# Performance work log

Measured on AMD Instinct MI355X. Metric: run time of the kernel, lower is better.

Reference implementation:

```python
import jax, jax.numpy as jnp
import numpy as np

N_NODES = 80000
N_EDGES = 1280000
IN_CH = 128
OUT_CH = 32
HID = 2 * OUT_CH


def gcn_conv(x, W, b, src, dst, n_nodes):
    """PyG GCNConv with self-loops and symmetric normalization.
    out[i] = b + sum_{j->i} deg(j)^-1/2 deg(i)^-1/2 (x_j @ W)
    """
    loop = jnp.arange(n_nodes, dtype=src.dtype)
    s = jnp.concatenate([src, loop])  # [E+N]
    d = jnp.concatenate([dst, loop])  # [E+N]
    deg = jax.ops.segment_sum(jnp.ones_like(d, dtype=x.dtype), d,
                              num_segments=n_nodes)  # in-degree incl. self loop
    dinv = jnp.where(deg > 0, jax.lax.rsqrt(deg), 0.0)
    norm = dinv[s] * dinv[d]  # [E+N]
    h = x @ W  # [N, F_out] dense transform first (fewer flops when F_out < F_in)
    msg = h[s] * norm[:, None]  # [E+N, F_out] gather + scale
    out = jax.ops.segment_sum(msg, d, num_segments=n_nodes)  # scatter-add
    return out + b


def setup_inputs() -> dict:
    key = jax.random.key(0)
    k1, k2, k3, k4 = jax.random.split(key, 4)
    x = jax.random.normal(k1, (N_NODES, IN_CH), dtype=jnp.float32)
    edge_index = jax.random.randint(k2, (2, N_EDGES), 0, N_NODES, dtype=jnp.int64)
    W1 = jax.random.normal(k3, (IN_CH, HID), dtype=jnp.float32) / np.sqrt(IN_CH)
    b1 = jnp.zeros((HID,), dtype=jnp.float32)
    W2 = jax.random.normal(k4, (HID, OUT_CH), dtype=jnp.float32) / np.sqrt(HID)
    b2 = jnp.zeros((OUT_CH,), dtype=jnp.float32)
    return {"x": x, "edge_index": edge_index, "W1": W1, "b1": b1,
            "W2": W2, "b2": b2}


def reference(x, edge_index, W1, b1, W2, b2):
    src, dst = edge_index[0], edge_index[1]
    h = jax.nn.relu(gcn_conv(x, W1, b1, src, dst, N_NODES))
    return gcn_conv(h, W2, b2, src, dst, N_NODES)
```

## Files before the change

### kernel.cpp

```cpp
#include <hip/hip_runtime.h>
#include <hip/hip_fp16.h>

#define N_NODES 80000
#define N_EDGES 1280000
#define IN_CH 128
#define HID 64
#define OUT_CH 32

#define NBUCK 625
#define CAP 3072
#define BIN_BLOCKS 256

typedef float vf2 __attribute__((ext_vector_type(2)));
typedef float vf4 __attribute__((ext_vector_type(4)));
typedef short short8 __attribute__((ext_vector_type(8)));
typedef float floatx4 __attribute__((ext_vector_type(4)));

__device__ __forceinline__ unsigned bf16rn(float x) {
    unsigned u = __float_as_uint(x);
    return (u + 0x7FFFu + ((u >> 16) & 1u)) >> 16;
}
__device__ __forceinline__ unsigned packbf2(float a, float b) {
    return bf16rn(a) | (bf16rn(b) << 16);
}
__device__ __forceinline__ float hl(unsigned u) {
    return __half2float(__ushort_as_half((unsigned short)(u & 0xFFFFu)));
}
__device__ __forceinline__ float hh(unsigned u) {
    return __half2float(__ushort_as_half((unsigned short)(u >> 16)));
}
__device__ __forceinline__ unsigned pack2h(float a, float b) {
    return (unsigned)__half_as_ushort(__float2half_rn(a)) |
           ((unsigned)__half_as_ushort(__float2half_rn(b)) << 16);
}

__global__ __launch_bounds__(256) void k_bin_gemm1(
        const int* __restrict__ src, const int* __restrict__ dst,
        int* __restrict__ gcur, unsigned int* __restrict__ binned,
        const float* __restrict__ x, const float* __restrict__ W1,
        unsigned short* __restrict__ h1h) {
    __shared__ unsigned short smem_u[26112];
    int bid = blockIdx.x, t = threadIdx.x;
    if (bid < BIN_BLOCKS) {
        int* hist = (int*)smem_u;
        int* lcur = hist + NBUCK;
        const int chunk = N_EDGES / BIN_BLOCKS;
        int e0 = bid * chunk;
        int e1 = e0 + chunk;
        for (int i = t; i < NBUCK; i += 256) hist[i] = 0;
        __syncthreads();
        for (int e = e0 + t; e < e1; e += 256)
            atomicAdd(&hist[dst[e] >> 7], 1);
        __syncthreads();
        for (int i = t; i < NBUCK; i += 256) {
            int h = hist[i];
            lcur[i] = h ? atomicAdd(&gcur[i], h) : 0;
        }
        __syncthreads();
        for (int e = e0 + t; e < e1; e += 256) {
            int d = dst[e];
            int bk = d >> 7;
            int pos = atomicAdd(&lcur[bk], 1);
            if (pos < CAP)
                binned[(size_t)bk * CAP + pos] =
                    (unsigned int)src[e] | ((unsigned int)(d & 127) << 17);
        }
    } else {
        unsigned short* sX = smem_u;
        unsigned short* sWT = smem_u + 128 * 136;
        long long nb = (long long)(bid - BIN_BLOCKS) * 128;
        for (int it = 0; it < 16; ++it) {
            int idx = t + it * 256;
            int node = idx >> 5, k4 = (idx & 31) * 4;
            float4 v = *(const float4*)&x[(nb + node) * IN_CH + k4];
            unsigned u0 = packbf2(v.x, v.y), u1 = packbf2(v.z, v.w);
            *(uint2*)&sX[node * 136 + k4] = (uint2){u0, u1};
        }
        for (int it = 0; it < 8; ++it) {
            int idx = t + it * 256;
            int k = idx >> 4, c4 = (idx & 15) * 4;
            float4 w = *(const float4*)&W1[k * 64 + c4];
            sWT[(c4 + 0) * 136 + k] = (unsigned short)bf16rn(w.x);
            sWT[(c4 + 1) * 136 + k] = (unsigned short)bf16rn(w.y);
            sWT[(c4 + 2) * 136 + k] = (unsigned short)bf16rn(w.z);
            sWT[(c4 + 3) * 136 + k] = (unsigned short)bf16rn(w.w);
        }
        __syncthreads();
        int wv = t >> 6, lane = t & 63;
        int lm = lane & 15, q = lane >> 4;
        int m0 = wv * 32;
        floatx4 acc[2][4];
#pragma unroll
        for (int i = 0; i < 2; ++i)
#pragma unroll
            for (int j = 0; j < 4; ++j) acc[i][j] = (floatx4){0.f, 0.f, 0.f, 0.f};
#pragma unroll
        for (int kk = 0; kk < 128; kk += 32) {
            short8 a0 = *(short8*)&sX[(m0 + lm) * 136 + kk + q * 8];
            short8 a1 = *(short8*)&sX[(m0 + 16 + lm) * 136 + kk + q * 8];
#pragma unroll
            for (int ct = 0; ct < 4; ++ct) {
                short8 bfr = *(short8*)&sWT[(ct * 16 + lm) * 136 + kk + q * 8];
                acc[0][ct] = __builtin_amdgcn_mfma_f32_16x16x32_bf16(a0, bfr, acc[0][ct], 0, 0, 0);
                acc[1][ct] = __builtin_amdgcn_mfma_f32_16x16x32_bf16(a1, bfr, acc[1][ct], 0, 0, 0);
            }
        }
#pragma unroll
        for (int mt = 0; mt < 2; ++mt)
#pragma unroll
            for (int ct = 0; ct < 4; ++ct)
#pragma unroll
                for (int r = 0; r < 4; ++r) {
                    long long node = nb + m0 + mt * 16 + q * 4 + r;
                    int c = ct * 16 + lm;
                    h1h[node * 64 + c] = __half_as_ushort(__float2half_rn(acc[mt][ct][r]));
                }
    }
}

__global__ __launch_bounds__(256) void k_csr(const unsigned int* __restrict__ binned,
                                             const int* __restrict__ cnt,
                                             int* __restrict__ csr,
                                             int2* __restrict__ rse,
                                             float* __restrict__ dinv,
                                             unsigned int* __restrict__ h1u) {
    __shared__ int deg[128];
    __shared__ int scan[128];
    __shared__ int cur[128];
    __shared__ float sdinv[128];
    int bk = blockIdx.x, t = threadIdx.x;
    int n_e = min(cnt[bk], CAP);
    const unsigned int* eb = binned + (size_t)bk * CAP;
    if (t < 128) deg[t] = 0;
    __syncthreads();
    for (int i = t; i < n_e; i += 256) atomicAdd(&deg[eb[i] >> 17], 1);
    __syncthreads();
    if (t < 128) scan[t] = deg[t];
    __syncthreads();
    for (int off = 1; off < 128; off <<= 1) {
        int v = (t < 128 && t >= off) ? scan[t - off] : 0;
        __syncthreads();
        if (t < 128) scan[t] += v;
        __syncthreads();
    }
    if (t < 128) {
        int incl = scan[t];
        int s = incl - deg[t];
        cur[t] = s;
        int n = bk * 128 + t;
        int base = bk * CAP;
        rse[n] = make_int2(base + s, base + incl);
        float dv = rsqrtf((float)(deg[t] + 1));
        dinv[n] = dv;
        sdinv[t] = dv;
    }
    __syncthreads();
    if (t < 32) {
        int p = n_e + t;
        if (p < CAP) csr[(size_t)bk * CAP + p] = 0;
    }
    for (int i = t; i < n_e; i += 256) {
        unsigned int p = eb[i];
        int dL = p >> 17;
        int pos = atomicAdd(&cur[dL], 1);
        csr[bk * CAP + pos] = (int)(p & 0x1FFFF);
    }
    size_t rbase = (size_t)bk * 128 * 32;
    for (int i = t; i < 128 * 16; i += 256) {
        int row = i >> 4, c = i & 15;
        uint2 u = *(uint2*)&h1u[rbase + (size_t)row * 32 + 2 * c];
        float dv = sdinv[row];
        u.x = pack2h(dv * hl(u.x), dv * hh(u.x));
        u.y = pack2h(dv * hl(u.y), dv * hh(u.y));
        *(uint2*)&h1u[rbase + (size_t)row * 32 + 2 * c] = u;
    }
}

__global__ __launch_bounds__(256) void k_agg64(
        const unsigned int* __restrict__ h1u, const int* __restrict__ csr,
        const int2* __restrict__ rse, const float* __restrict__ dinv,
        const float* __restrict__ b1, const float* __restrict__ W2,
        unsigned int* __restrict__ g2u) {
    __shared__ float sW2[64 * 32];
    __shared__ float sH2[4][2][64];
    int t = threadIdx.x;
    for (int i = t * 2; i < 64 * 32; i += 512)
        *(vf2*)&sW2[i] = *(const vf2*)&W2[i];

    int wv = t >> 6, lane = t & 63;
    int nd = lane >> 5;
    int q  = (lane >> 4) & 1;
    int fo = lane & 15;
    int col = lane & 31;
    int n = blockIdx.x * 8 + wv * 2 + nd;

    int2 rb = rse[n];
    float dn = dinv[n];
    uint2 un = *(const uint2*)&h1u[(size_t)n * 32 + 2 * fo];
    float4 bb = *(const float4*)&b1[4 * fo];
    int a = rb.x, b = rb.y;
    int e0 = a + q;
    int ss[12];
#pragma unroll
    for (int i = 0; i < 12; ++i) ss[i] = csr[e0 + 2 * i];
#pragma unroll
    for (int i = 1; i < 12; ++i) ss[i] = (e0 + 2 * i < b) ? ss[i] : ss[0];
    float ax = 0.f, ay = 0.f, az = 0.f, aw = 0.f;
#pragma unroll
    for (int i = 0; i < 12; ++i) {
        uint2 u = *(const uint2*)&h1u[(size_t)ss[i] * 32 + 2 * fo];
        if (e0 + 2 * i < b) {
            ax += hl(u.x); ay += hh(u.x); az += hl(u.y); aw += hh(u.y);
        }
    }
    for (int e = e0 + 24; e < b; e += 2) {
        int s = csr[e];
        uint2 u = *(const uint2*)&h1u[(size_t)s * 32 + 2 * fo];
        ax += hl(u.x); ay += hh(u.x); az += hl(u.y); aw += hh(u.y);
    }
    ax += __shfl_down(ax, 16); ay += __shfl_down(ay, 16);
    az += __shfl_down(az, 16); aw += __shfl_down(aw, 16);
    __syncthreads();
    if (q == 0) {
        ax += hl(un.x); ay += hh(un.x); az += hl(un.y); aw += hh(un.y);
        vf4 h2v = {fmaxf(dn * ax + bb.x, 0.f), fmaxf(dn * ay + bb.y, 0.f),
                   fmaxf(dn * az + bb.z, 0.f), fmaxf(dn * aw + bb.w, 0.f)};
        *(vf4*)&sH2[wv][nd][4 * fo] = h2v;
    }
    __syncthreads();
    int nd2 = lane >> 5;
    const float* hrow = sH2[wv][nd2];
    float g = 0.f;
#pragma unroll
    for (int k = 0; k < 64; ++k) g += hrow[k] * sW2[k * 32 + col];
    g *= dn;
    float g1 = __shfl_down(g, 1);
    float g2v = __shfl_down(g, 2);
    float g3v = __shfl_down(g, 3);
    if ((lane & 3) == 0) {
        uint2 p = {pack2h(g, g1), pack2h(g2v, g3v)};
        *(uint2*)&g2u[(size_t)n * 16 + (col >> 1)] = p;
    }
}

__global__ __launch_bounds__(256) void k_agg32(
        const unsigned int* __restrict__ g2u, const int* __restrict__ csr,
        const int2* __restrict__ rse, const float* __restrict__ dinv,
        const float* __restrict__ b2, float* __restrict__ outp) {
    int n = blockIdx.x * 4 + (threadIdx.x >> 6);
    int lane = threadIdx.x & 63;
    int oc = lane >> 3, fo = lane & 7;
    int2 rb = rse[n];
    float dn = dinv[n];
    uint2 un = *(const uint2*)&g2u[(size_t)n * 16 + 2 * fo];
    int a = rb.x, b = rb.y;
    int e0 = a + oc;
    int s0 = csr[e0];
    int s1 = csr[e0 + 8];
    int s2 = csr[e0 + 16];
    s1 = (e0 + 8  < b) ? s1 : s0;
    s2 = (e0 + 16 < b) ? s2 : s0;
    float ax = 0.f, ay = 0.f, az = 0.f, aw = 0.f;
    uint2 u0 = *(const uint2*)&g2u[(size_t)s0 * 16 + 2 * fo];
    uint2 u1 = *(const uint2*)&g2u[(size_t)s1 * 16 + 2 * fo];
    uint2 u2 = *(const uint2*)&g2u[(size_t)s2 * 16 + 2 * fo];
    if (e0 < b)      { ax += hl(u0.x); ay += hh(u0.x); az += hl(u0.y); aw += hh(u0.y); }
    if (e0 + 8 < b)  { ax += hl(u1.x); ay += hh(u1.x); az += hl(u1.y); aw += hh(u1.y); }
    if (e0 + 16 < b) { ax += hl(u2.x); ay += hh(u2.x); az += hl(u2.y); aw += hh(u2.y); }
    for (int e = e0 + 24; e < b; e += 8) {
        int s = csr[e];
        uint2 u = *(const uint2*)&g2u[(size_t)s * 16 + 2 * fo];
        ax += hl(u.x); ay += hh(u.x); az += hl(u.y); aw += hh(u.y);
    }
    ax += __shfl_down(ax, 32); ay += __shfl_down(ay, 32);
    az += __shfl_down(az, 32); aw += __shfl_down(aw, 32);
    ax += __shfl_down(ax, 16); ay += __shfl_down(ay, 16);
    az += __shfl_down(az, 16); aw += __shfl_down(aw, 16);
    ax += __shfl_down(ax, 8);  ay += __shfl_down(ay, 8);
    az += __shfl_down(az, 8);  aw += __shfl_down(aw, 8);
    if (oc == 0) {
        ax += hl(un.x); ay += hh(un.x);
        az += hl(un.y); aw += hh(un.y);
        float4 bbv = *(const float4*)&b2[4 * fo];
        vf4 o = {dn * ax + bbv.x, dn * ay + bbv.y, dn * az + bbv.z, dn * aw + bbv.w};
        __builtin_nontemporal_store(o, (vf4*)&outp[(size_t)n * 32 + 4 * fo]);
    }
}

static inline size_t align256(size_t x) { return (x + 255) & ~(size_t)255; }

extern "C" void kernel_launch(void* const* d_in, const int* in_sizes, int n_in,
                              void* d_out, int out_size, void* d_ws, size_t ws_size,
                              hipStream_t stream) {
    const float* x  = (const float*)d_in[0];
    const int*   ei = (const int*)d_in[1];
    const float* W1 = (const float*)d_in[2];
    const float* b1 = (const float*)d_in[3];
    const float* W2 = (const float*)d_in[4];
    const float* b2 = (const float*)d_in[5];
    float* out = (float*)d_out;

    const int* src = ei;
    const int* dst = ei + N_EDGES;

    char* ws = (char*)d_ws;
    size_t off = 0;
    int* gcur = (int*)(ws + off);              off = align256(off + NBUCK * 4);
    unsigned int* binned = (unsigned int*)(ws + off);
                                               off = align256(off + (size_t)NBUCK * CAP * 4);
    int* csr = (int*)(ws + off);               off = align256(off + (size_t)NBUCK * CAP * 4 + 128);
    int2* rse = (int2*)(ws + off);             off = align256(off + (size_t)N_NODES * 8);
    float* dinv = (float*)(ws + off);          off = align256(off + (size_t)N_NODES * 4);
    unsigned short* h1h = (unsigned short*)(ws + off);
                                               off = align256(off + (size_t)N_NODES * 64 * 2);
    unsigned int* g2u = (unsigned int*)(ws + off);
                                               off = align256(off + (size_t)N_NODES * 16 * 4);

    (void)hipMemsetAsync(gcur, 0, NBUCK * 4, stream);
    k_bin_gemm1<<<BIN_BLOCKS + N_NODES / 128, 256, 0, stream>>>(src, dst, gcur, binned,
                                                                x, W1, h1h);
    k_csr<<<NBUCK, 256, 0, stream>>>(binned, gcur, csr, rse, dinv,
                                     (unsigned int*)h1h);
    k_agg64<<<N_NODES / 8, 256, 0, stream>>>((const unsigned int*)h1h, csr, rse,
                                             dinv, b1, W2, g2u);
    k_agg32<<<N_NODES / 4, 256, 0, stream>>>(g2u, csr, rse, dinv, b2, out);
}
```

Measured before the change: 202.0 us.

## Add padded ELL neighbor table with zero sentinel row for aggregation kernels

```diff
diff --git a/kernel.cpp b/kernel.cpp
--- a/kernel.cpp
+++ b/kernel.cpp
@@ -10,6 +10,7 @@
 #define NBUCK 625
 #define CAP 3072
 #define BIN_BLOCKS 256
+#define ELLW 24
 
 typedef float vf2 __attribute__((ext_vector_type(2)));
 typedef float vf4 __attribute__((ext_vector_type(4)));
@@ -121,12 +122,14 @@
 __global__ __launch_bounds__(256) void k_csr(const unsigned int* __restrict__ binned,
                                              const int* __restrict__ cnt,
                                              int* __restrict__ csr,
+                                             int* __restrict__ ell,
                                              int2* __restrict__ rse,
-                                             float* __restrict__ dinv,
+                                             float2* __restrict__ meta,
                                              unsigned int* __restrict__ h1u) {
     __shared__ int deg[128];
     __shared__ int scan[128];
     __shared__ int cur[128];
+    __shared__ int rst[128];
     __shared__ float sdinv[128];
     int bk = blockIdx.x, t = threadIdx.x;
     int n_e = min(cnt[bk], CAP);
@@ -147,23 +150,25 @@
         int incl = scan[t];
         int s = incl - deg[t];
         cur[t] = s;
+        rst[t] = s;
         int n = bk * 128 + t;
         int base = bk * CAP;
         rse[n] = make_int2(base + s, base + incl);
         float dv = rsqrtf((float)(deg[t] + 1));
-        dinv[n] = dv;
+        meta[n] = make_float2(dv, (float)deg[t]);
         sdinv[t] = dv;
     }
-    __syncthreads();
-    if (t < 32) {
-        int p = n_e + t;
-        if (p < CAP) csr[(size_t)bk * CAP + p] = 0;
-    }
+    int* eb_ell = ell + (size_t)bk * 128 * ELLW;
+    for (int i = t; i < 128 * ELLW; i += 256) eb_ell[i] = N_NODES;
+    __syncthreads();
     for (int i = t; i < n_e; i += 256) {
         unsigned int p = eb[i];
         int dL = p >> 17;
         int pos = atomicAdd(&cur[dL], 1);
-        csr[bk * CAP + pos] = (int)(p & 0x1FFFF);
+        int s = (int)(p & 0x1FFFF);
+        csr[bk * CAP + pos] = s;
+        int lp = pos - rst[dL];
+        if (lp < ELLW) eb_ell[dL * ELLW + lp] = s;
     }
     size_t rbase = (size_t)bk * 128 * 32;
     for (int i = t; i < 128 * 16; i += 256) {
@@ -177,10 +182,10 @@
 }
 
 __global__ __launch_bounds__(256) void k_agg64(
-        const unsigned int* __restrict__ h1u, const int* __restrict__ csr,
-        const int2* __restrict__ rse, const float* __restrict__ dinv,
-        const float* __restrict__ b1, const float* __restrict__ W2,
-        unsigned int* __restrict__ g2u) {
+        const unsigned int* __restrict__ h1u, const int* __restrict__ ell,
+        const int* __restrict__ csr, const int2* __restrict__ rse,
+        const float2* __restrict__ meta, const float* __restrict__ b1,
+        const float* __restrict__ W2, unsigned int* __restrict__ g2u) {
     __shared__ float sW2[64 * 32];
     __shared__ float sH2[4][2][64];
     int t = threadIdx.x;
@@ -194,29 +199,38 @@
     int col = lane & 31;
     int n = blockIdx.x * 8 + wv * 2 + nd;
 
-    int2 rb = rse[n];
-    float dn = dinv[n];
+    float2 mt = meta[n];
+    float dn = mt.x;
+    int dg = (int)mt.y;
     uint2 un = *(const uint2*)&h1u[(size_t)n * 32 + 2 * fo];
     float4 bb = *(const float4*)&b1[4 * fo];
-    int a = rb.x, b = rb.y;
-    int e0 = a + q;
+    const int* er = ell + (size_t)n * ELLW;
+    int4 w0 = *(const int4*)&er[0];
+    int4 w1 = *(const int4*)&er[4];
+    int4 w2 = *(const int4*)&er[8];
+    int4 w3 = *(const int4*)&er[12];
+    int4 w4 = *(const int4*)&er[16];
+    int4 w5 = *(const int4*)&er[20];
     int ss[12];
-#pragma unroll
-    for (int i = 0; i < 12; ++i) ss[i] = csr[e0 + 2 * i];
-#pragma unroll
-    for (int i = 1; i < 12; ++i) ss[i] = (e0 + 2 * i < b) ? ss[i] : ss[0];
+    ss[0]  = q ? w0.y : w0.x;  ss[1]  = q ? w0.w : w0.z;
+    ss[2]  = q ? w1.y : w1.x;  ss[3]  = q ? w1.w : w1.z;
+    ss[4]  = q ? w2.y : w2.x;  ss[5]  = q ? w2.w : w2.z;
+    ss[6]  = q ? w3.y : w3.x;  ss[7]  = q ? w3.w : w3.z;
+    ss[8]  = q ? w4.y : w4.x;  ss[9]  = q ? w4.w : w4.z;
+    ss[10] = q ? w5.y : w5.x;  ss[11] = q ? w5.w : w5.z;
     float ax = 0.f, ay = 0.f, az = 0.f, aw = 0.f;
 #pragma unroll
     for (int i = 0; i < 12; ++i) {
         uint2 u = *(const uint2*)&h1u[(size_t)ss[i] * 32 + 2 * fo];
-        if (e0 + 2 * i < b) {
+        ax += hl(u.x); ay += hh(u.x); az += hl(u.y); aw += hh(u.y);
+    }
+    if (dg > ELLW) {
+        int2 rb = rse[n];
+        for (int e = rb.x + ELLW + q; e < rb.y; e += 2) {
+            int s = csr[e];
+            uint2 u = *(const uint2*)&h1u[(size_t)s * 32 + 2 * fo];
             ax += hl(u.x); ay += hh(u.x); az += hl(u.y); aw += hh(u.y);
         }
-    }
-    for (int e = e0 + 24; e < b; e += 2) {
-        int s = csr[e];
-        uint2 u = *(const uint2*)&h1u[(size_t)s * 32 + 2 * fo];
-        ax += hl(u.x); ay += hh(u.x); az += hl(u.y); aw += hh(u.y);
     }
     ax += __shfl_down(ax, 16); ay += __shfl_down(ay, 16);
     az += __shfl_down(az, 16); aw += __shfl_down(aw, 16);
@@ -244,33 +258,35 @@
 }
 
 __global__ __launch_bounds__(256) void k_agg32(
-        const unsigned int* __restrict__ g2u, const int* __restrict__ csr,
-        const int2* __restrict__ rse, const float* __restrict__ dinv,
-        const float* __restrict__ b2, float* __restrict__ outp) {
+        const unsigned int* __restrict__ g2u, const int* __restrict__ ell,
+        const int* __restrict__ csr, const int2* __restrict__ rse,
+        const float2* __restrict__ meta, const float* __restrict__ b2,
+        float* __restrict__ outp) {
     int n = blockIdx.x * 4 + (threadIdx.x >> 6);
     int lane = threadIdx.x & 63;
     int oc = lane >> 3, fo = lane & 7;
-    int2 rb = rse[n];
-    float dn = dinv[n];
+    float2 mt = meta[n];
+    float dn = mt.x;
+    int dg = (int)mt.y;
     uint2 un = *(const uint2*)&g2u[(size_t)n * 16 + 2 * fo];
-    int a = rb.x, b = rb.y;
-    int e0 = a + oc;
-    int s0 = csr[e0];
-    int s1 = csr[e0 + 8];
-    int s2 = csr[e0 + 16];
-    s1 = (e0 + 8  < b) ? s1 : s0;
-    s2 = (e0 + 16 < b) ? s2 : s0;
-    float ax = 0.f, ay = 0.f, az = 0.f, aw = 0.f;
+    const int* er = ell + (size_t)n * ELLW;
+    int s0 = er[oc];
+    int s1 = er[oc + 8];
+    int s2 = er[oc + 16];
     uint2 u0 = *(const uint2*)&g2u[(size_t)s0 * 16 + 2 * fo];
     uint2 u1 = *(const uint2*)&g2u[(size_t)s1 * 16 + 2 * fo];
     uint2 u2 = *(const uint2*)&g2u[(size_t)s2 * 16 + 2 * fo];
-    if (e0 < b)      { ax += hl(u0.x); ay += hh(u0.x); az += hl(u0.y); aw += hh(u0.y); }
-    if (e0 + 8 < b)  { ax += hl(u1.x); ay += hh(u1.x); az += hl(u1.y); aw += hh(u1.y); }
-    if (e0 + 16 < b) { ax += hl(u2.x); ay += hh(u2.x); az += hl(u2.y); aw += hh(u2.y); }
-    for (int e = e0 + 24; e < b; e += 8) {
-        int s = csr[e];
-        uint2 u = *(const uint2*)&g2u[(size_t)s * 16 + 2 * fo];
-        ax += hl(u.x); ay += hh(u.x); az += hl(u.y); aw += hh(u.y);
+    float ax, ay, az, aw;
+    ax  = hl(u0.x); ay  = hh(u0.x); az  = hl(u0.y); aw  = hh(u0.y);
+    ax += hl(u1.x); ay += hh(u1.x); az += hl(u1.y); aw += hh(u1.y);
+    ax += hl(u2.x); ay += hh(u2.x); az += hl(u2.y); aw += hh(u2.y);
+    if (dg > ELLW) {
+        int2 rb = rse[n];
+        for (int e = rb.x + ELLW + oc; e < rb.y; e += 8) {
+            int s = csr[e];
+            uint2 u = *(const uint2*)&g2u[(size_t)s * 16 + 2 * fo];
+            ax += hl(u.x); ay += hh(u.x); az += hl(u.y); aw += hh(u.y);
+        }
     }
     ax += __shfl_down(ax, 32); ay += __shfl_down(ay, 32);
     az += __shfl_down(az, 32); aw += __shfl_down(aw, 32);
@@ -308,20 +324,23 @@
     int* gcur = (int*)(ws + off);              off = align256(off + NBUCK * 4);
     unsigned int* binned = (unsigned int*)(ws + off);
                                                off = align256(off + (size_t)NBUCK * CAP * 4);
-    int* csr = (int*)(ws + off);               off = align256(off + (size_t)NBUCK * CAP * 4 + 128);
+    int* csr = (int*)(ws + off);               off = align256(off + (size_t)NBUCK * CAP * 4);
+    int* ell = (int*)(ws + off);               off = align256(off + (size_t)N_NODES * ELLW * 4);
     int2* rse = (int2*)(ws + off);             off = align256(off + (size_t)N_NODES * 8);
-    float* dinv = (float*)(ws + off);          off = align256(off + (size_t)N_NODES * 4);
+    float2* meta = (float2*)(ws + off);        off = align256(off + (size_t)N_NODES * 8);
     unsigned short* h1h = (unsigned short*)(ws + off);
-                                               off = align256(off + (size_t)N_NODES * 64 * 2);
+                                               off = align256(off + (size_t)(N_NODES + 1) * 64 * 2);
     unsigned int* g2u = (unsigned int*)(ws + off);
-                                               off = align256(off + (size_t)N_NODES * 16 * 4);
+                                               off = align256(off + (size_t)(N_NODES + 1) * 16 * 4);
 
     (void)hipMemsetAsync(gcur, 0, NBUCK * 4, stream);
+    (void)hipMemsetAsync(h1h + (size_t)N_NODES * 64, 0, 64 * 2, stream);
+    (void)hipMemsetAsync(g2u + (size_t)N_NODES * 16, 0, 16 * 4, stream);
     k_bin_gemm1<<<BIN_BLOCKS + N_NODES / 128, 256, 0, stream>>>(src, dst, gcur, binned,
                                                                 x, W1, h1h);
-    k_csr<<<NBUCK, 256, 0, stream>>>(binned, gcur, csr, rse, dinv,
+    k_csr<<<NBUCK, 256, 0, stream>>>(binned, gcur, csr, ell, rse, meta,
                                      (unsigned int*)h1h);
-    k_agg64<<<N_NODES / 8, 256, 0, stream>>>((const unsigned int*)h1h, csr, rse,
-                                             dinv, b1, W2, g2u);
-    k_agg32<<<N_NODES / 4, 256, 0, stream>>>(g2u, csr, rse, dinv, b2, out);
-}
+    k_agg64<<<N_NODES / 8, 256, 0, stream>>>((const unsigned int*)h1h, ell, csr, rse,
+                                             meta, b1, W2, g2u);
+    k_agg32<<<N_NODES / 4, 256, 0, stream>>>(g2u, ell, csr, rse, meta, b2, out);
+}
```

New measurement: 204.7 us. About the same (+1.3%).
